# Performance work log

Measured on AMD Instinct MI355X. Metric: run time of the kernel, lower is better.

The kernel has to match this reference:

```python
import jax, jax.numpy as jnp
from jax import lax
import numpy as np

NE = 8          # ne_num
IDX_REF = 4     # ne_num // 2
EPS_BN = 1e-5


def conv2d(x, w, b=None, pad=0):
    out = lax.conv_general_dilated(x, w, (1, 1), [(pad, pad), (pad, pad)],
                                   dimension_numbers=('NCHW', 'OIHW', 'NCHW'))
    if b is not None:
        out = out + b[None, :, None, None]
    return out


def bn(x, gamma, beta):
    # training-mode batch norm (biased variance), as nn.BatchNorm2d in train()
    mu = x.mean(axis=(0, 2, 3), keepdims=True)
    var = x.var(axis=(0, 2, 3), keepdims=True)
    xn = (x - mu) * lax.rsqrt(var + EPS_BN)
    return xn * gamma[None, :, None, None] + beta[None, :, None, None]


def gauss_win(sigma):
    # sigma: (B,1). window_size=3 -> bias = [-1, 0, -1]; pop center of 3x3 -> (B,8)
    bias = jnp.array([-1.0, 0.0, -1.0], dtype=sigma.dtype)
    g = jnp.exp(bias[None, :] / (2.0 * sigma ** 2))            # (B,3)
    w1 = g / g.sum(axis=1, keepdims=True)                      # (B,3)
    w2 = (w1[:, :, None] * w1[:, None, :]).reshape(-1, 9)      # (B,9)
    return jnp.concatenate([w2[:, :4], w2[:, 5:]], axis=1)     # (B,8) center removed


def bilinear(img, y, x):
    # img: (B,H,W); y,x: (B,K,H,W) float sample coords; zero padding outside
    B, H, W = img.shape
    y0 = jnp.floor(y); x0 = jnp.floor(x)
    wy1 = y - y0; wy0 = 1.0 - wy1
    wx1 = x - x0; wx0 = 1.0 - wx1
    imgf = img.reshape(B, -1)

    def gather(yi, xi):
        yii = yi.astype(jnp.int32); xii = xi.astype(jnp.int32)
        valid = (yii >= 0) & (yii < H) & (xii >= 0) & (xii < W)
        idx = jnp.clip(yii, 0, H - 1) * W + jnp.clip(xii, 0, W - 1)
        v = jnp.take_along_axis(imgf, idx.reshape(B, -1), axis=1).reshape(idx.shape)
        return jnp.where(valid, v, 0.0)

    return (wy0 * wx0 * gather(y0, x0) + wy0 * wx1 * gather(y0, x0 + 1.0)
            + wy1 * wx0 * gather(y0 + 1.0, x0) + wy1 * wx1 * gather(y0 + 1.0, x0 + 1.0))


def modulated_deform_conv_1x9(fusion, offset, mask):
    # ModulatedDeformConvFunction with weight=ones(1,1,3,3), bias=0, stride=1,
    # pad=1, dilation=1, groups=1, deformable_groups=1.
    # fusion: (B,1,H,W); offset: (B,9,2,H,W) [per-neighbor (dy,dx)]; mask: (B,9,H,W)
    B, _, H, W = fusion.shape
    k = jnp.arange(9)
    py = (k // 3 - 1).astype(fusion.dtype)[None, :, None, None]
    px = (k % 3 - 1).astype(fusion.dtype)[None, :, None, None]
    hh = jnp.arange(H, dtype=fusion.dtype)[None, None, :, None]
    ww = jnp.arange(W, dtype=fusion.dtype)[None, None, None, :]
    y = hh + py + offset[:, :, 0]
    x = ww + px + offset[:, :, 1]
    samp = bilinear(fusion[:, 0], y, x)            # (B,9,H,W)
    return (mask * samp).sum(axis=1, keepdims=True)  # (B,1,H,W)


def _forward(feat, g1_w, g1_g, g1_b, g2_w, g2_g, g2_b, g3_w, g3_bias,
             f1_w, f1_g, f1_b, f2_w, f2_bias,
             s1_w, s1_b, s2_w, s2_b, s3_w, s3_b,
             oa1_w, oa1_g, oa1_b, oa2_w, oa2_g, oa2_b, oa3_w, oa3_bias,
             aff_scale):
    B, _, H, W = feat.shape
    # guid branch (5x5 convs)
    guid = jax.nn.relu(bn(conv2d(feat, g1_w, pad=2), g1_g, g1_b))
    guid = jax.nn.relu(bn(conv2d(guid, g2_w, pad=2), g2_g, g2_b))
    guid = conv2d(guid, g3_w, g3_bias, pad=2)                      # (B,8,H,W)
    # fuse branch
    f = jax.nn.relu(bn(conv2d(feat, f1_w, pad=1), f1_g, f1_b))
    fusion = jnp.tanh(conv2d(f, f2_w, f2_bias, pad=1))             # (B,1,H,W)
    # sigma branch (CAM, detached input)
    fd = lax.stop_gradient(feat)
    p = fd.mean(axis=(2, 3))                                       # (B,32)
    h = jax.nn.celu(p @ s1_w.T + s1_b)
    h = jax.nn.celu(h @ s2_w.T + s2_b)
    sigma = jax.nn.relu(h @ s3_w.T + s3_b) + 0.001                 # (B,1)
    # get_off_aff(guid, sigma, sigma_gamma=0.2, window_size=3)
    oa = jax.nn.relu(bn(conv2d(guid, oa1_w, pad=2), oa1_g, oa1_b))
    oa = jax.nn.relu(bn(conv2d(oa, oa2_w, pad=2), oa2_g, oa2_b))
    oa = conv2d(oa, oa3_w, oa3_bias, pad=2)                        # (B,24,H,W)
    o1, o2, affc = jnp.split(oa, 3, axis=1)                        # each (B,8,H,W)
    off = jnp.concatenate([o1, o2], axis=1).reshape(B, NE, 2, H, W)
    zero_ref = jnp.zeros((B, 1, 2, H, W), dtype=off.dtype)
    offset = jnp.concatenate([off[:, :IDX_REF], zero_ref, off[:, IDX_REF:]], axis=1)  # (B,9,2,H,W)
    gk = gauss_win(sigma + 0.2)                                    # (B,8)
    aff = jnp.tanh(affc) / (aff_scale + 1e-5) + gk[:, :, None, None]
    sa = jnp.abs(aff).sum(axis=1, keepdims=True) + 1e-5
    sa = jnp.maximum(sa, 1.0)
    aff = aff / sa
    aff_ref = 1.0 - aff.sum(axis=1, keepdims=True)
    aff9 = jnp.concatenate([aff[:, :IDX_REF], aff_ref, aff[:, IDX_REF:]], axis=1)  # (B,9,H,W)
    # gauss_filter (times=1) + abs
    gfusion = jnp.abs(modulated_deform_conv_1x9(fusion, offset, aff9))
    return gfusion


def setup_inputs() -> dict:
    key = jax.random.key(0)
    ks = list(jax.random.split(key, 32))
    B, C, H, W = 8, 32, 320, 320
    ne = NE
    d = {}
    d['feat'] = jax.random.normal(ks[0], (B, C, H, W), jnp.float32)

    def wconv(k, o, i, s):
        return jax.random.normal(k, (o, i, s, s), jnp.float32) * (1.0 / np.sqrt(i * s * s))

    def wlin(k, o, i):
        return jax.random.normal(k, (o, i), jnp.float32) * (1.0 / np.sqrt(i))

    # guid: 32->32 (5), 32->8 (5), 8->8 (5, bias)
    d['g1_w'] = wconv(ks[1], C, C, 5); d['g1_g'] = jnp.ones(C) + 0.1 * jax.random.normal(ks[2], (C,)); d['g1_b'] = 0.1 * jax.random.normal(ks[3], (C,))
    d['g2_w'] = wconv(ks[4], ne, C, 5); d['g2_g'] = jnp.ones(ne) + 0.1 * jax.random.normal(ks[5], (ne,)); d['g2_b'] = 0.1 * jax.random.normal(ks[6], (ne,))
    d['g3_w'] = wconv(ks[7], ne, ne, 5); d['g3_bias'] = 0.1 * jax.random.normal(ks[8], (ne,))
    # fuse: 32->32 (3), 32->1 (3, bias)
    d['f1_w'] = wconv(ks[9], C, C, 3); d['f1_g'] = jnp.ones(C) + 0.1 * jax.random.normal(ks[10], (C,)); d['f1_b'] = 0.1 * jax.random.normal(ks[11], (C,))
    d['f2_w'] = wconv(ks[12], 1, C, 3); d['f2_bias'] = 0.1 * jax.random.normal(ks[13], (1,))
    # gen_sigma CAM: 32->16->16->1
    d['s1_w'] = wlin(ks[14], 16, C); d['s1_b'] = 0.1 * jax.random.normal(ks[15], (16,))
    d['s2_w'] = wlin(ks[16], 16, 16); d['s2_b'] = 0.1 * jax.random.normal(ks[17], (16,))
    d['s3_w'] = wlin(ks[18], 1, 16); d['s3_b'] = 0.1 * jax.random.normal(ks[19], (1,))
    # conv_off_aff: 8->8 (5), 8->24 (5), 24->24 (5, bias)
    d['oa1_w'] = wconv(ks[20], ne, ne, 5); d['oa1_g'] = jnp.ones(ne) + 0.1 * jax.random.normal(ks[21], (ne,)); d['oa1_b'] = 0.1 * jax.random.normal(ks[22], (ne,))
    d['oa2_w'] = wconv(ks[23], 3 * ne, ne, 5); d['oa2_g'] = jnp.ones(3 * ne) + 0.1 * jax.random.normal(ks[24], (3 * ne,)); d['oa2_b'] = 0.1 * jax.random.normal(ks[25], (3 * ne,))
    d['oa3_w'] = wconv(ks[26], 3 * ne, 3 * ne, 5); d['oa3_bias'] = 0.1 * jax.random.normal(ks[27], (3 * ne,))
    # aff_scale_const = aff_gamma * ne_num = 0.5 * 8
    d['aff_scale'] = jnp.full((1,), 4.0, jnp.float32)
    return d


def reference(feat, g1_w, g1_g, g1_b, g2_w, g2_g, g2_b, g3_w, g3_bias,
              f1_w, f1_g, f1_b, f2_w, f2_bias,
              s1_w, s1_b, s2_w, s2_b, s3_w, s3_b,
              oa1_w, oa1_g, oa1_b, oa2_w, oa2_g, oa2_b, oa3_w, oa3_bias,
              aff_scale):
    return _forward(feat, g1_w, g1_g, g1_b, g2_w, g2_g, g2_b, g3_w, g3_bias,
                    f1_w, f1_g, f1_b, f2_w, f2_bias,
                    s1_w, s1_b, s2_w, s2_b, s3_w, s3_b,
                    oa1_w, oa1_g, oa1_b, oa2_w, oa2_g, oa2_b, oa3_w, oa3_bias,
                    aff_scale)
```

## Files before the change

### kernel.cpp

```cpp
#include <hip/hip_runtime.h>
#include <hip/hip_bf16.h>
#include <math.h>

#define B_   8
#define H_   320
#define W_   320
#define HW_  (320*320)

typedef __attribute__((ext_vector_type(8))) short bf16x8;
typedef __attribute__((ext_vector_type(4))) short bf16x4s;
typedef __attribute__((ext_vector_type(4))) float f32x4;

__device__ __forceinline__ short f2b(float v){
    __hip_bfloat16 h = __float2bfloat16(v);
    return *(short*)&h;
}
__device__ __forceinline__ float bf2f(short v){
    unsigned u = ((unsigned)(unsigned short)v) << 16;
    return __uint_as_float(u);
}

__global__ void convert_k(const float* __restrict__ in, short* __restrict__ out,
                          float* __restrict__ psum){
    const int b  = blockIdx.y;
    const int px = blockIdx.x*256 + threadIdx.x;
    const float* src = in + (long)b*32*HW_ + px;
    short* dst = out + ((long)b*HW_ + px)*32;
    float f[32];
    short v[32];
    #pragma unroll
    for (int c=0;c<32;++c){ f[c] = src[(long)c*HW_]; v[c] = f2b(f[c]); }
    #pragma unroll
    for (int s=0;s<4;++s)
        *(bf16x8*)(dst + s*8) = *(bf16x8*)(v + s*8);
    #pragma unroll
    for (int c=0;c<32;++c){
        float s = f[c];
        #pragma unroll
        for (int o=1;o<64;o<<=1) s += __shfl_xor(s, o, 64);
        f[c] = s;
    }
    __shared__ float red[4][32];
    const int lane = threadIdx.x & 63, wid = threadIdx.x >> 6;
    if (lane < 32) red[wid][lane] = f[lane];
    __syncthreads();
    if (threadIdx.x < 32)
        atomicAdd(&psum[b*32 + threadIdx.x],
                  red[0][threadIdx.x]+red[1][threadIdx.x]+red[2][threadIdx.x]+red[3][threadIdx.x]);
}

__global__ void repack_k(const float* __restrict__ sf1, const float* __restrict__ sf2,
                         const float* __restrict__ sg1, const float* __restrict__ sg2,
                         const float* __restrict__ sg3, const float* __restrict__ so1,
                         const float* __restrict__ so2, const float* __restrict__ so3,
                         short* __restrict__ dst){
    const int cum[8]  = {9216,13824,39424,52224,55808,59392,66560,92160};
    const int CINs[8] = {32,32,32,32, 8, 8, 8,24};
    const int CIps[8] = {32,32,32,32, 8, 8, 8,32};
    const int COUTs[8]= {32, 1,32, 8, 8, 8,24,24};
    const int MTs[8]  = { 2, 1, 2, 1, 1, 1, 2, 2};
    const int Ks[8]   = { 3, 3, 5, 5, 5, 5, 5, 5};
    int i = blockIdx.x*256 + threadIdx.x;
    if (i >= 92160) return;
    int s = 0;
    while (i >= cum[s]) ++s;
    const int base = s ? cum[s-1] : 0;
    const int il = i - base;
    const float* src = (s==0)?sf1:(s==1)?sf2:(s==2)?sg1:(s==3)?sg2:(s==4)?sg3:(s==5)?so1:(s==6)?so2:so3;
    const int kl   = il & 31;
    const int co_l = (il >> 5) & 15;
    const int rem  = il >> 9;
    const int MT = MTs[s];
    const int mt = rem % MT;
    const int c  = rem / MT;
    const int K = Ks[s];
    int tap, ci;
    if (CIps[s] == 32){ tap = (c % K)*K + (c / K); ci = kl; }
    else              { tap = c*4 + (kl>>3); ci = kl & 7; }
    const int co = mt*16 + co_l;
    float v = 0.f;
    if (co < COUTs[s] && ci < CINs[s] && tap < K*K){
        const int ky = tap / K, kx = tap - ky*K;
        v = src[((co*CINs[s] + ci)*K + ky)*K + kx];
    }
    dst[i] = f2b(v);
}

__device__ __forceinline__
float deform_px(const float* val, const float* __restrict__ fus_b,
                const float* __restrict__ gk_b, float inv_s, int y, int x){
    float aff[8]; float sa = 0.f;
    #pragma unroll
    for (int n=0;n<8;++n){
        float a = tanhf(val[16+n]) * inv_s + gk_b[n];
        aff[n] = a; sa += fabsf(a);
    }
    sa += 1e-5f;
    sa = fmaxf(sa, 1.f);
    const float isa = 1.f/sa;
    float ssum = 0.f;
    #pragma unroll
    for (int n=0;n<8;++n){ aff[n] *= isa; ssum += aff[n]; }
    const float aff_ref = 1.f - ssum;

    float o = 0.f;
    #pragma unroll
    for (int k=0;k<9;++k){
        float dy, dx, m;
        if (k == 4){ dy = 0.f; dx = 0.f; m = aff_ref; }
        else {
            const int n = (k < 4) ? k : k-1;
            dy = val[2*n];
            dx = val[2*n+1];
            m  = aff[n];
        }
        float yy = (float)(y + k/3 - 1) + dy;
        float xx = (float)(x + k%3 - 1) + dx;
        float y0f = floorf(yy), x0f = floorf(xx);
        int   y0 = (int)y0f,    x0i = (int)x0f;
        float wy1 = yy - y0f, wy0 = 1.f - wy1;
        float wx1 = xx - x0f, wx0 = 1.f - wx1;
        float v00 = (y0  >=0 && y0  <H_ && x0i  >=0 && x0i  <W_) ? fus_b[ y0   *W_ + x0i  ] : 0.f;
        float v01 = (y0  >=0 && y0  <H_ && x0i+1>=0 && x0i+1<W_) ? fus_b[ y0   *W_ + x0i+1] : 0.f;
        float v10 = (y0+1>=0 && y0+1<H_ && x0i  >=0 && x0i  <W_) ? fus_b[(y0+1)*W_ + x0i  ] : 0.f;
        float v11 = (y0+1>=0 && y0+1<H_ && x0i+1>=0 && x0i+1<W_) ? fus_b[(y0+1)*W_ + x0i+1] : 0.f;
        o += m * (wy0*(wx0*v00 + wx1*v01) + wy1*(wx0*v10 + wx1*v11));
    }
    return fabsf(o);
}

template<int CIN, int CIp, int COUT, int MT, int K,
         bool IN_BN, bool OUT_STATS, int OUT_MODE, int OCP>
__global__ __launch_bounds__(256, 4)
void mconv_k(const void* __restrict__ inv,
             const float* __restrict__ bn_sum, const float* __restrict__ bn_sq,
             const float* __restrict__ gamma, const float* __restrict__ beta,
             const short* __restrict__ wr, const float* __restrict__ bias,
             void* __restrict__ outv,
             float* __restrict__ osum, float* __restrict__ osq,
             const float* __restrict__ fus, const float* __restrict__ gk,
             const float* __restrict__ aff_scale){
    constexpr int PAD = K/2;
    constexpr int TH  = 8;
    constexpr int LW  = 32 + K - 1;
    constexpr int LH  = TH + K - 1;
    constexpr int SEGS = CIp/8;
    constexpr int PLANE = LH*LW*8 + 8;
    constexpr int NTAPS  = K*K;
    constexpr int NCHUNK = (CIp==32) ? NTAPS : (NTAPS*CIp + 31)/32;
    constexpr int INB  = (CIp==32) ? (SEGS*PLANE*2) : (LH*LW*8*2);
    constexpr int DUMPB = 256*25*4;
    constexpr int LDSB = (OUT_MODE==3 && INB < DUMPB) ? DUMPB : INB;

    __shared__ __align__(16) char ldsraw[LDSB];
    short* lds_in = (short*)ldsraw;
    __shared__ float sc_sh[2][32];
    __shared__ float red[2][4][32];

    const int tid = threadIdx.x;
    const int b   = blockIdx.z;
    const int x0  = blockIdx.x*32, y0 = blockIdx.y*TH;

    const int lane = tid & 63;
    const int wv   = tid >> 6;
    const int pxn  = lane & 15;
    const int quad = lane >> 4;
    const int row0 = 2*wv;

    if (IN_BN){
        if (tid < 32){
            float s = 1.f, sh2 = 0.f;
            if (tid < CIN){
                const float invN = 1.f/(float)(B_*HW_);
                float mu  = bn_sum[tid]*invN;
                float var = bn_sq[tid]*invN - mu*mu;
                s   = gamma[tid] * rsqrtf(var + 1e-5f);
                sh2 = beta[tid] - mu*s;
            }
            sc_sh[0][tid] = s;
            sc_sh[1][tid] = sh2;
        }
        __syncthreads();
    }

    constexpr int KC = (CIp==32) ? K : 1;
    bf16x8 aC[KC][MT];
    bf16x8 aAll[(CIp==8)?NCHUNK:1][MT];

    if constexpr (CIp == 32){
        #pragma unroll
        for (int ky=0; ky<K; ++ky)
            #pragma unroll
            for (int m=0;m<MT;++m)
                aC[ky][m] = *(const bf16x8*)(wr + ((ky*MT + m)*16 + pxn)*32 + quad*8);
    } else {
        #pragma unroll
        for (int c=0;c<NCHUNK;++c)
            #pragma unroll
            for (int m=0;m<MT;++m)
                aAll[c][m] = *(const bf16x8*)(wr + (((c*MT + m)*16 + pxn)*32 + quad*8));
    }

    {
        const short* src = (const short*)inv + (long)b*HW_*CIp;
        constexpr int NU = LH*LW*SEGS;
        constexpr int NIT = (NU + 255)/256;
        bf16x8 vv[NIT];
        int    la[NIT];
        bool   ib[NIT];
        #pragma unroll
        for (int it=0; it<NIT; ++it){
            const int u = tid + it*256;
            bf16x8 v = {0,0,0,0,0,0,0,0};
            bool inb = false;
            int addr = 0;
            if (u < NU){
                const int r   = u / (LW*SEGS);
                const int rem = u - r*(LW*SEGS);
                const int xl  = rem / SEGS;
                const int seg = rem - xl*SEGS;
                const int gy = y0 + r - PAD, gx = x0 + xl - PAD;
                addr = seg*PLANE + (r*LW + xl)*8;
                inb = (gy>=0 && gy<H_ && gx>=0 && gx<W_);
                if (inb)
                    v = *(const bf16x8*)(src + ((long)gy*W_ + gx)*CIp + seg*8);
            }
            vv[it] = v; la[it] = addr; ib[it] = inb;
        }
        __builtin_amdgcn_sched_barrier(0);
        #pragma unroll
        for (int it=0; it<NIT; ++it){
            const int u = tid + it*256;
            if (u < NU){
                bf16x8 v = vv[it];
                if (IN_BN && ib[it]){
                    const int seg = u - (u/SEGS)*SEGS;
                    #pragma unroll
                    for (int j=0;j<8;++j){
                        float f = bf2f(v[j]);
                        f = fmaxf(fmaf(f, sc_sh[0][seg*8+j], sc_sh[1][seg*8+j]), 0.f);
                        v[j] = f2b(f);
                    }
                }
                *(bf16x8*)&lds_in[la[it]] = v;
            }
        }
    }
    __syncthreads();

    const f32x4 zero = {0.f, 0.f, 0.f, 0.f};
    f32x4 acc[2][MT][2];
    #pragma unroll
    for (int rr=0;rr<2;++rr)
        #pragma unroll
        for (int m=0;m<MT;++m){ acc[rr][m][0] = zero; acc[rr][m][1] = zero; }

    if constexpr (CIp == 32){
        const short* bbase = lds_in + quad*PLANE + (row0*LW + pxn)*8;
        #pragma unroll
        for (int kx=0; kx<K; ++kx){
            bf16x8 bw[3][2];
            #pragma unroll
            for (int r=0;r<2;++r)
                #pragma unroll
                for (int n=0;n<2;++n)
                    bw[r][n] = *(const bf16x8*)(bbase + (r*LW + kx + n*16)*8);
            __builtin_amdgcn_sched_barrier(0);
            #pragma unroll
            for (int ky=0; ky<K; ++ky){
                if (ky < K-1){
                    #pragma unroll
                    for (int n=0;n<2;++n)
                        bw[(ky+2)%3][n] = *(const bf16x8*)(bbase + ((ky+2)*LW + kx + n*16)*8);
                }
                __builtin_amdgcn_sched_barrier(0);
                #pragma unroll
                for (int m=0;m<MT;++m){
                    acc[0][m][0] = __builtin_amdgcn_mfma_f32_16x16x32_bf16(aC[ky][m], bw[ky%3][0],     acc[0][m][0], 0,0,0);
                    acc[0][m][1] = __builtin_amdgcn_mfma_f32_16x16x32_bf16(aC[ky][m], bw[ky%3][1],     acc[0][m][1], 0,0,0);
                    acc[1][m][0] = __builtin_amdgcn_mfma_f32_16x16x32_bf16(aC[ky][m], bw[(ky+1)%3][0], acc[1][m][0], 0,0,0);
                    acc[1][m][1] = __builtin_amdgcn_mfma_f32_16x16x32_bf16(aC[ky][m], bw[(ky+1)%3][1], acc[1][m][1], 0,0,0);
                }
                if (kx+1 < K){
                    #pragma unroll
                    for (int m=0;m<MT;++m)
                        aC[ky][m] = *(const bf16x8*)(wr + ((((kx+1)*K+ky)*MT + m)*16 + pxn)*32 + quad*8);
                }
            }
        }
    } else {
        auto bptr = [&](int c, int rr)->const short*{
            const int row = row0 + rr;
            int t = c*4 + quad;
            if (t >= NTAPS) t = 0;
            const int ky = t / K, kx = t - ky*K;
            return lds_in + ((row+ky)*LW + kx + pxn)*8;
        };

        bf16x8 bcp[2][2][2];
        #pragma unroll
        for (int rr=0;rr<2;++rr){
            const short* bp = bptr(0, rr);
            bcp[0][rr][0] = *(const bf16x8*)bp;
            bcp[0][rr][1] = *(const bf16x8*)(bp + 16*8);
        }

        #pragma unroll
        for (int c=0; c<NCHUNK; ++c){
            if (c+1 < NCHUNK){
                #pragma unroll
                for (int rr=0;rr<2;++rr){
                    const short* bpn = bptr(c+1, rr);
                    bcp[(c+1)&1][rr][0] = *(const bf16x8*)bpn;
                    bcp[(c+1)&1][rr][1] = *(const bf16x8*)(bpn + 16*8);
                }
            }
            __builtin_amdgcn_sched_barrier(0);
            #pragma unroll
            for (int m=0;m<MT;++m)
                #pragma unroll
                for (int rr=0;rr<2;++rr){
                    acc[rr][m][0] = __builtin_amdgcn_mfma_f32_16x16x32_bf16(aAll[c][m], bcp[c&1][rr][0], acc[rr][m][0], 0,0,0);
                    acc[rr][m][1] = __builtin_amdgcn_mfma_f32_16x16x32_bf16(aAll[c][m], bcp[c&1][rr][1], acc[rr][m][1], 0,0,0);
                }
        }
    }

    if (OUT_STATS){
        #pragma unroll
        for (int m=0;m<MT;++m){
            #pragma unroll
            for (int r=0;r<4;++r){
                float v  = acc[0][m][0][r] + acc[0][m][1][r]
                         + acc[1][m][0][r] + acc[1][m][1][r];
                float v2 = acc[0][m][0][r]*acc[0][m][0][r] + acc[0][m][1][r]*acc[0][m][1][r]
                         + acc[1][m][0][r]*acc[1][m][0][r] + acc[1][m][1][r]*acc[1][m][1][r];
                #pragma unroll
                for (int o=1;o<16;o<<=1){
                    v  += __shfl_xor(v,  o, 64);
                    v2 += __shfl_xor(v2, o, 64);
                }
                if (pxn == 0){
                    red[0][wv][m*16 + quad*4 + r] = v;
                    red[1][wv][m*16 + quad*4 + r] = v2;
                }
            }
        }
        __syncthreads();
        if (tid < MT*16 && tid < COUT){
            atomicAdd(&osum[tid], red[0][0][tid]+red[0][1][tid]+red[0][2][tid]+red[0][3][tid]);
            atomicAdd(&osq[tid],  red[1][0][tid]+red[1][1][tid]+red[1][2][tid]+red[1][3][tid]);
        }
    }

    if (OUT_MODE == 3){
        float* out = (float*)outv;
        __syncthreads();
        float* dumpf = (float*)ldsraw;
        #pragma unroll
        for (int rr=0;rr<2;++rr){
            const int row = row0 + rr;
            #pragma unroll
            for (int m=0;m<MT;++m){
                if (m*16 + quad*4 < 24){
                    #pragma unroll
                    for (int n=0;n<2;++n)
                        #pragma unroll
                        for (int r=0;r<4;++r)
                            dumpf[(row*32 + n*16 + pxn)*25 + (m*16 + quad*4 + r)] = acc[rr][m][n][r];
                }
            }
        }
        __syncthreads();
        {
            float val[24];
            #pragma unroll
            for (int c2=0;c2<24;++c2) val[c2] = dumpf[tid*25 + c2] + bias[c2];
            const int yy = y0 + (tid>>5), xx = x0 + (tid&31);
            const float inv_s = 1.f/(aff_scale[0] + 1e-5f);
            out[(long)b*HW_ + yy*W_ + xx] =
                deform_px(val, fus + (long)b*HW_, gk + b*8, inv_s, yy, xx);
        }
    } else if (OUT_MODE == 2){
        float* out = (float*)outv;
        #pragma unroll
        for (int rr=0;rr<2;++rr){
            const int y = y0 + row0 + rr;
            #pragma unroll
            for (int m=0;m<MT;++m){
                #pragma unroll
                for (int r=0;r<4;++r){
                    const int co = m*16 + quad*4 + r;
                    if (co < COUT){
                        float* op = out + (((long)b*COUT + co)*H_ + y)*W_ + x0;
                        #pragma unroll
                        for (int n=0;n<2;++n)
                            op[n*16 + pxn] = tanhf(acc[rr][m][n][r] + bias[co]);
                    }
                }
            }
        }
    } else {
        short* o = (short*)outv;
        #pragma unroll
        for (int rr=0;rr<2;++rr){
            const int y = y0 + row0 + rr;
            #pragma unroll
            for (int m=0;m<MT;++m){
                const int co0 = m*16 + quad*4;
                if (co0 < OCP){
                    #pragma unroll
                    for (int n=0;n<2;++n){
                        bf16x4s pk;
                        #pragma unroll
                        for (int r=0;r<4;++r){
                            float f = acc[rr][m][n][r];
                            if (OUT_MODE == 1) f += bias[co0+r];
                            pk[r] = f2b(f);
                        }
                        const long px = ((long)b*H_ + y)*W_ + x0 + n*16 + pxn;
                        *(bf16x4s*)(o + px*OCP + co0) = pk;
                    }
                }
            }
        }
    }
}

template<int KK, int OFF>
__device__ __forceinline__
void conv_core32(const short* __restrict__ lds_in, const short* __restrict__ wr,
                 int row0, int pxn, int quad, f32x4 acc[2][2][2]){
    constexpr int LW = 36;
    constexpr int PLANE = 12*36*8 + 8;
    const short* bbase = lds_in + quad*PLANE + ((row0+OFF)*LW + OFF + pxn)*8;
    bf16x8 aC[KK][2];
    #pragma unroll
    for (int ky=0; ky<KK; ++ky)
        #pragma unroll
        for (int m=0;m<2;++m)
            aC[ky][m] = *(const bf16x8*)(wr + ((ky*2 + m)*16 + pxn)*32 + quad*8);
    #pragma unroll
    for (int kx=0; kx<KK; ++kx){
        bf16x8 bw[3][2];
        #pragma unroll
        for (int r=0;r<2;++r)
            #pragma unroll
            for (int n=0;n<2;++n)
                bw[r][n] = *(const bf16x8*)(bbase + (r*LW + kx + n*16)*8);
        __builtin_amdgcn_sched_barrier(0);
        #pragma unroll
        for (int ky=0; ky<KK; ++ky){
            if (ky < KK-1){
                #pragma unroll
                for (int n=0;n<2;++n)
                    bw[(ky+2)%3][n] = *(const bf16x8*)(bbase + ((ky+2)*LW + kx + n*16)*8);
            }
            __builtin_amdgcn_sched_barrier(0);
            #pragma unroll
            for (int m=0;m<2;++m){
                acc[0][m][0] = __builtin_amdgcn_mfma_f32_16x16x32_bf16(aC[ky][m], bw[ky%3][0],     acc[0][m][0], 0,0,0);
                acc[0][m][1] = __builtin_amdgcn_mfma_f32_16x16x32_bf16(aC[ky][m], bw[ky%3][1],     acc[0][m][1], 0,0,0);
                acc[1][m][0] = __builtin_amdgcn_mfma_f32_16x16x32_bf16(aC[ky][m], bw[(ky+1)%3][0], acc[1][m][0], 0,0,0);
                acc[1][m][1] = __builtin_amdgcn_mfma_f32_16x16x32_bf16(aC[ky][m], bw[(ky+1)%3][1], acc[1][m][1], 0,0,0);
            }
            if (kx+1 < KK){
                #pragma unroll
                for (int m=0;m<2;++m)
                    aC[ky][m] = *(const bf16x8*)(wr + ((((kx+1)*KK+ky)*2 + m)*16 + pxn)*32 + quad*8);
            }
        }
    }
}

__global__ __launch_bounds__(256, 4)
void mconv_fg_k(const short* __restrict__ feat,
                const short* __restrict__ wf, const short* __restrict__ wg,
                short* __restrict__ f1o, short* __restrict__ g1o,
                float* __restrict__ sum0, float* __restrict__ sq0,
                float* __restrict__ sum1, float* __restrict__ sq1){
    constexpr int PAD = 2, LW = 36, LH = 12, SEGS = 4;
    constexpr int PLANE = LH*LW*8 + 8;

    __shared__ __align__(16) char ldsraw[SEGS*PLANE*2];
    short* lds_in = (short*)ldsraw;
    __shared__ float red[2][4][32];

    const int tid = threadIdx.x;
    const int b   = blockIdx.z;
    const int x0  = blockIdx.x*32, y0 = blockIdx.y*8;

    const int lane = tid & 63;
    const int wv   = tid >> 6;
    const int pxn  = lane & 15;
    const int quad = lane >> 4;
    const int row0 = 2*wv;

    {
        const short* src = feat + (long)b*HW_*32;
        constexpr int NU = LH*LW*SEGS;
        constexpr int NIT = (NU + 255)/256;
        bf16x8 vv[NIT];
        int    la[NIT];
        #pragma unroll
        for (int it=0; it<NIT; ++it){
            const int u = tid + it*256;
            bf16x8 v = {0,0,0,0,0,0,0,0};
            int addr = 0;
            if (u < NU){
                const int r   = u / (LW*SEGS);
                const int rem = u - r*(LW*SEGS);
                const int xl  = rem / SEGS;
                const int seg = rem - xl*SEGS;
                const int gy = y0 + r - PAD, gx = x0 + xl - PAD;
                addr = seg*PLANE + (r*LW + xl)*8;
                if (gy>=0 && gy<H_ && gx>=0 && gx<W_)
                    v = *(const bf16x8*)(src + ((long)gy*W_ + gx)*32 + seg*8);
            }
            vv[it] = v; la[it] = addr;
        }
        __builtin_amdgcn_sched_barrier(0);
        #pragma unroll
        for (int it=0; it<NIT; ++it){
            if (tid + it*256 < NU)
                *(bf16x8*)&lds_in[la[it]] = vv[it];
        }
    }
    __syncthreads();

    const f32x4 zero = {0.f, 0.f, 0.f, 0.f};
    f32x4 acc[2][2][2];

    #pragma unroll
    for (int rr=0;rr<2;++rr)
        #pragma unroll
        for (int m=0;m<2;++m){ acc[rr][m][0] = zero; acc[rr][m][1] = zero; }
    conv_core32<3,1>(lds_in, wf, row0, pxn, quad, acc);
    #pragma unroll
    for (int m=0;m<2;++m)
        #pragma unroll
        for (int r=0;r<4;++r){
            float v  = acc[0][m][0][r] + acc[0][m][1][r] + acc[1][m][0][r] + acc[1][m][1][r];
            float v2 = acc[0][m][0][r]*acc[0][m][0][r] + acc[0][m][1][r]*acc[0][m][1][r]
                     + acc[1][m][0][r]*acc[1][m][0][r] + acc[1][m][1][r]*acc[1][m][1][r];
            #pragma unroll
            for (int o=1;o<16;o<<=1){ v += __shfl_xor(v, o, 64); v2 += __shfl_xor(v2, o, 64); }
            if (pxn == 0){ red[0][wv][m*16+quad*4+r] = v; red[1][wv][m*16+quad*4+r] = v2; }
        }
    __syncthreads();
    if (tid < 32){
        atomicAdd(&sum0[tid], red[0][0][tid]+red[0][1][tid]+red[0][2][tid]+red[0][3][tid]);
        atomicAdd(&sq0[tid],  red[1][0][tid]+red[1][1][tid]+red[1][2][tid]+red[1][3][tid]);
    }
    #pragma unroll
    for (int rr=0;rr<2;++rr){
        const int y = y0 + row0 + rr;
        #pragma unroll
        for (int m=0;m<2;++m){
            const int co0 = m*16 + quad*4;
            #pragma unroll
            for (int n=0;n<2;++n){
                bf16x4s pk;
                #pragma unroll
                for (int r=0;r<4;++r) pk[r] = f2b(acc[rr][m][n][r]);
                const long px = ((long)b*H_ + y)*W_ + x0 + n*16 + pxn;
                *(bf16x4s*)(f1o + px*32 + co0) = pk;
            }
        }
    }
    __syncthreads();

    #pragma unroll
    for (int rr=0;rr<2;++rr)
        #pragma unroll
        for (int m=0;m<2;++m){ acc[rr][m][0] = zero; acc[rr][m][1] = zero; }
    conv_core32<5,0>(lds_in, wg, row0, pxn, quad, acc);
    #pragma unroll
    for (int m=0;m<2;++m)
        #pragma unroll
        for (int r=0;r<4;++r){
            float v  = acc[0][m][0][r] + acc[0][m][1][r] + acc[1][m][0][r] + acc[1][m][1][r];
            float v2 = acc[0][m][0][r]*acc[0][m][0][r] + acc[0][m][1][r]*acc[0][m][1][r]
                     + acc[1][m][0][r]*acc[1][m][0][r] + acc[1][m][1][r]*acc[1][m][1][r];
            #pragma unroll
            for (int o=1;o<16;o<<=1){ v += __shfl_xor(v, o, 64); v2 += __shfl_xor(v2, o, 64); }
            if (pxn == 0){ red[0][wv][m*16+quad*4+r] = v; red[1][wv][m*16+quad*4+r] = v2; }
        }
    __syncthreads();
    if (tid < 32){
        atomicAdd(&sum1[tid], red[0][0][tid]+red[0][1][tid]+red[0][2][tid]+red[0][3][tid]);
        atomicAdd(&sq1[tid],  red[1][0][tid]+red[1][1][tid]+red[1][2][tid]+red[1][3][tid]);
    }
    #pragma unroll
    for (int rr=0;rr<2;++rr){
        const int y = y0 + row0 + rr;
        #pragma unroll
        for (int m=0;m<2;++m){
            const int co0 = m*16 + quad*4;
            #pragma unroll
            for (int n=0;n<2;++n){
                bf16x4s pk;
                #pragma unroll
                for (int r=0;r<4;++r) pk[r] = f2b(acc[rr][m][n][r]);
                const long px = ((long)b*H_ + y)*W_ + x0 + n*16 + pxn;
                *(bf16x4s*)(g1o + px*32 + co0) = pk;
            }
        }
    }
}

__global__ void sigma_k(const float* __restrict__ p,
                        const float* s1w, const float* s1b,
                        const float* s2w, const float* s2b,
                        const float* s3w, const float* s3b,
                        float* __restrict__ gk){
    const int b = threadIdx.x;
    if (b >= B_) return;
    float pb[32];
    for (int j=0;j<32;++j) pb[j] = p[b*32+j] * (1.f/(float)HW_);
    float h1[16], h2[16];
    for (int i=0;i<16;++i){
        float t = s1b[i];
        for (int j=0;j<32;++j) t = fmaf(pb[j], s1w[i*32+j], t);
        h1[i] = t > 0.f ? t : expm1f(t);
    }
    for (int i=0;i<16;++i){
        float t = s2b[i];
        for (int j=0;j<16;++j) t = fmaf(h1[j], s2w[i*16+j], t);
        h2[i] = t > 0.f ? t : expm1f(t);
    }
    float t = s3b[0];
    for (int j=0;j<16;++j) t = fmaf(h2[j], s3w[j], t);
    float sigma = fmaxf(t, 0.f) + 0.001f;
    float sg = sigma + 0.2f;
    float e = expf(-1.f/(2.f*sg*sg));
    float inv = 1.f/(2.f*e + 1.f);
    float a = e*inv, c = inv;
    float* g = gk + b*8;
    g[0]=a*a; g[1]=a*c; g[2]=a*a; g[3]=c*a; g[4]=c*a; g[5]=a*a; g[6]=a*c; g[7]=a*a;
}

extern "C" void kernel_launch(void* const* d_in, const int* in_sizes, int n_in,
                              void* d_out, int out_size, void* d_ws, size_t ws_size,
                              hipStream_t stream){
    const float* feat    = (const float*)d_in[0];
    const float* g1_w    = (const float*)d_in[1];
    const float* g1_g    = (const float*)d_in[2];
    const float* g1_b    = (const float*)d_in[3];
    const float* g2_w    = (const float*)d_in[4];
    const float* g2_g    = (const float*)d_in[5];
    const float* g2_b    = (const float*)d_in[6];
    const float* g3_w    = (const float*)d_in[7];
    const float* g3_bias = (const float*)d_in[8];
    const float* f1_w    = (const float*)d_in[9];
    const float* f1_g    = (const float*)d_in[10];
    const float* f1_b    = (const float*)d_in[11];
    const float* f2_w    = (const float*)d_in[12];
    const float* f2_bias = (const float*)d_in[13];
    const float* s1w     = (const float*)d_in[14];
    const float* s1b     = (const float*)d_in[15];
    const float* s2w     = (const float*)d_in[16];
    const float* s2b     = (const float*)d_in[17];
    const float* s3w     = (const float*)d_in[18];
    const float* s3b     = (const float*)d_in[19];
    const float* oa1_w   = (const float*)d_in[20];
    const float* oa1_g   = (const float*)d_in[21];
    const float* oa1_b   = (const float*)d_in[22];
    const float* oa2_w   = (const float*)d_in[23];
    const float* oa2_g   = (const float*)d_in[24];
    const float* oa2_b   = (const float*)d_in[25];
    const float* oa3_w   = (const float*)d_in[26];
    const float* oa3_bias= (const float*)d_in[27];
    const float* aff_scale=(const float*)d_in[28];
    float* out = (float*)d_out;

    char* ws = (char*)d_ws;
    short* FEAT = (short*)(ws + 0L);
    short* A1   = (short*)(ws + 52428800L);
    short* A2   = (short*)(ws + 104857600L);
    short* GUID = (short*)(ws + 117964800L);
    float* FUS  = (float*)(ws + 131072000L);
    float* SM   = (float*)(ws + 134348800L);
    short* OA2  = A1;
    short* G1O  = (short*)(ws + 135266304L);
    const bool merged = (ws_size >= 135266304UL + 52428800UL);

    float* sum = SM;
    float* sq  = SM + 320;
    float* p   = SM + 640;
    float* gk  = SM + 896;
    short* WBs = (short*)(SM + 960);
    short* w_f1 = WBs + 0;
    short* w_f2 = WBs + 9216;
    short* w_g1 = WBs + 13824;
    short* w_g2 = WBs + 39424;
    short* w_g3 = WBs + 52224;
    short* w_o1 = WBs + 55808;
    short* w_o2 = WBs + 59392;
    short* w_o3 = WBs + 66560;

    hipMemsetAsync(sum, 0, 896*sizeof(float), stream);

    repack_k<<<dim3(360), dim3(256), 0, stream>>>(
        f1_w, f2_w, g1_w, g2_w, g3_w, oa1_w, oa2_w, oa3_w, WBs);
    convert_k<<<dim3(HW_/256, B_), dim3(256), 0, stream>>>(feat, FEAT, p);

    sigma_k<<<dim3(1), dim3(64), 0, stream>>>(p, s1w, s1b, s2w, s2b, s3w, s3b, gk);

    const dim3 cgrid(10, 40, 8), cblk(256);
    #define MCONV(CIN,CIp,COUT,MT,K,IBN,OST,OM,OCP) \
        mconv_k<CIN,CIp,COUT,MT,K,IBN,OST,OM,OCP><<<cgrid,cblk,0,stream>>>

    const short* G1SRC;
    if (merged){
        mconv_fg_k<<<cgrid, cblk, 0, stream>>>(FEAT, w_f1, w_g1, A1, G1O,
                                               sum+0*64, sq+0*64, sum+1*64, sq+1*64);
        MCONV(32,32, 1,1,3,true ,false,2, 0)(A1, sum+0*64, sq+0*64, f1_g, f1_b,
            w_f2, f2_bias, FUS, nullptr, nullptr, nullptr, nullptr, nullptr);
        G1SRC = G1O;
    } else {
        MCONV(32,32,32,2,3,false,true ,0,32)(FEAT, nullptr, nullptr, nullptr, nullptr,
            w_f1, nullptr, A1, sum+0*64, sq+0*64, nullptr, nullptr, nullptr);
        MCONV(32,32, 1,1,3,true ,false,2, 0)(A1, sum+0*64, sq+0*64, f1_g, f1_b,
            w_f2, f2_bias, FUS, nullptr, nullptr, nullptr, nullptr, nullptr);
        MCONV(32,32,32,2,5,false,true ,0,32)(FEAT, nullptr, nullptr, nullptr, nullptr,
            w_g1, nullptr, A1, sum+1*64, sq+1*64, nullptr, nullptr, nullptr);
        G1SRC = A1;
    }

    MCONV(32,32, 8,1,5,true ,true ,0, 8)(G1SRC, sum+1*64, sq+1*64, g1_g, g1_b,
        w_g2, nullptr, A2, sum+2*64, sq+2*64, nullptr, nullptr, nullptr);
    MCONV( 8, 8, 8,1,5,true ,false,1, 8)(A2, sum+2*64, sq+2*64, g2_g, g2_b,
        w_g3, g3_bias, GUID, nullptr, nullptr, nullptr, nullptr, nullptr);

    MCONV( 8, 8, 8,1,5,false,true ,0, 8)(GUID, nullptr, nullptr, nullptr, nullptr,
        w_o1, nullptr, A2, sum+3*64, sq+3*64, nullptr, nullptr, nullptr);
    MCONV( 8, 8,24,2,5,true ,true ,0,32)(A2, sum+3*64, sq+3*64, oa1_g, oa1_b,
        w_o2, nullptr, OA2, sum+4*64, sq+4*64, nullptr, nullptr, nullptr);
    MCONV(24,32,24,2,5,true ,false,3, 0)(OA2, sum+4*64, sq+4*64, oa2_g, oa2_b,
        w_o3, oa3_bias, out, nullptr, nullptr, FUS, gk, aff_scale);
    #undef MCONV
}
```

Before: 567.4 us.

## Fuse fp32-to-bf16 input conversion and channel pooling into merged first conv

Removes the separate convert_k pass. The merged f1/g1 conv kernel now reads fp32 NCHW features directly, converts them to bf16 into LDS, and accumulates per-channel sums for sigma through shared and global atomics. The G1O buffer moves to the start of the workspace, freed now that the FEAT staging buffer is gone, which lowers the workspace size needed to take the merged path. The cost is strided per-channel global loads (32 scattered reads per pixel) in place of 16-byte vector loads, plus many LDS atomics per block.

```diff
diff --git a/kernel.cpp b/kernel.cpp
--- a/kernel.cpp
+++ b/kernel.cpp
@@ -474,17 +474,19 @@
 }
 
 __global__ __launch_bounds__(256, 4)
-void mconv_fg_k(const short* __restrict__ feat,
+void mconv_fg_k(const float* __restrict__ featf,
                 const short* __restrict__ wf, const short* __restrict__ wg,
                 short* __restrict__ f1o, short* __restrict__ g1o,
                 float* __restrict__ sum0, float* __restrict__ sq0,
-                float* __restrict__ sum1, float* __restrict__ sq1){
-    constexpr int PAD = 2, LW = 36, LH = 12, SEGS = 4;
+                float* __restrict__ sum1, float* __restrict__ sq1,
+                float* __restrict__ psum){
+    constexpr int PAD = 2, LW = 36, LH = 12;
     constexpr int PLANE = LH*LW*8 + 8;
 
-    __shared__ __align__(16) char ldsraw[SEGS*PLANE*2];
+    __shared__ __align__(16) char ldsraw[4*PLANE*2];
     short* lds_in = (short*)ldsraw;
     __shared__ float red[2][4][32];
+    __shared__ float psl[32];
 
     const int tid = threadIdx.x;
     const int b   = blockIdx.z;
@@ -496,37 +498,44 @@
     const int quad = lane >> 4;
     const int row0 = 2*wv;
 
+    if (tid < 32) psl[tid] = 0.f;
+    __syncthreads();
+
     {
-        const short* src = feat + (long)b*HW_*32;
-        constexpr int NU = LH*LW*SEGS;
-        constexpr int NIT = (NU + 255)/256;
-        bf16x8 vv[NIT];
-        int    la[NIT];
-        #pragma unroll
-        for (int it=0; it<NIT; ++it){
-            const int u = tid + it*256;
-            bf16x8 v = {0,0,0,0,0,0,0,0};
-            int addr = 0;
-            if (u < NU){
-                const int r   = u / (LW*SEGS);
-                const int rem = u - r*(LW*SEGS);
-                const int xl  = rem / SEGS;
-                const int seg = rem - xl*SEGS;
-                const int gy = y0 + r - PAD, gx = x0 + xl - PAD;
-                addr = seg*PLANE + (r*LW + xl)*8;
-                if (gy>=0 && gy<H_ && gx>=0 && gx<W_)
-                    v = *(const bf16x8*)(src + ((long)gy*W_ + gx)*32 + seg*8);
-            }
-            vv[it] = v; la[it] = addr;
-        }
-        __builtin_amdgcn_sched_barrier(0);
-        #pragma unroll
-        for (int it=0; it<NIT; ++it){
-            if (tid + it*256 < NU)
-                *(bf16x8*)&lds_in[la[it]] = vv[it];
+        const float* srcb = featf + (long)b*32*HW_;
+        #pragma unroll
+        for (int it=0; it<2; ++it){
+            const int upx = tid + it*256;
+            const bool valid = upx < LH*LW;
+            const int r  = valid ? (upx / LW) : 0;
+            const int xl = upx - r*LW;
+            const int gy = y0 + r - PAD, gx = x0 + xl - PAD;
+            const bool inb = valid && gy>=0 && gy<H_ && gx>=0 && gx<W_;
+            float f[32];
+            if (inb){
+                const float* sp = srcb + (long)gy*W_ + gx;
+                #pragma unroll
+                for (int c=0;c<32;++c) f[c] = sp[(long)c*HW_];
+            } else {
+                #pragma unroll
+                for (int c=0;c<32;++c) f[c] = 0.f;
+            }
+            if (valid){
+                short v[32];
+                #pragma unroll
+                for (int c=0;c<32;++c) v[c] = f2b(f[c]);
+                #pragma unroll
+                for (int s=0;s<4;++s)
+                    *(bf16x8*)&lds_in[s*PLANE + (r*LW + xl)*8] = *(bf16x8*)(v + s*8);
+            }
+            if (valid && r>=PAD && r<PAD+8 && xl>=PAD && xl<PAD+32){
+                #pragma unroll
+                for (int c=0;c<32;++c) atomicAdd(&psl[c], f[c]);
+            }
         }
     }
     __syncthreads();
+    if (tid < 32) atomicAdd(&psum[b*32 + tid], psl[tid]);
 
     const f32x4 zero = {0.f, 0.f, 0.f, 0.f};
     f32x4 acc[2][2][2];
@@ -682,8 +691,8 @@
     float* FUS  = (float*)(ws + 131072000L);
     float* SM   = (float*)(ws + 134348800L);
     short* OA2  = A1;
-    short* G1O  = (short*)(ws + 135266304L);
-    const bool merged = (ws_size >= 135266304UL + 52428800UL);
+    short* G1O  = (short*)(ws + 0L);
+    const bool merged = (ws_size >= 134348800UL + 4096UL*400UL);
 
     float* sum = SM;
     float* sq  = SM + 320;
@@ -703,9 +712,6 @@
 
     repack_k<<<dim3(360), dim3(256), 0, stream>>>(
         f1_w, f2_w, g1_w, g2_w, g3_w, oa1_w, oa2_w, oa3_w, WBs);
-    convert_k<<<dim3(HW_/256, B_), dim3(256), 0, stream>>>(feat, FEAT, p);
-
-    sigma_k<<<dim3(1), dim3(64), 0, stream>>>(p, s1w, s1b, s2w, s2b, s3w, s3b, gk);
 
     const dim3 cgrid(10, 40, 8), cblk(256);
     #define MCONV(CIN,CIp,COUT,MT,K,IBN,OST,OM,OCP) \
@@ -713,12 +719,15 @@
 
     const short* G1SRC;
     if (merged){
-        mconv_fg_k<<<cgrid, cblk, 0, stream>>>(FEAT, w_f1, w_g1, A1, G1O,
-                                               sum+0*64, sq+0*64, sum+1*64, sq+1*64);
+        mconv_fg_k<<<cgrid, cblk, 0, stream>>>(feat, w_f1, w_g1, A1, G1O,
+                                               sum+0*64, sq+0*64, sum+1*64, sq+1*64, p);
+        sigma_k<<<dim3(1), dim3(64), 0, stream>>>(p, s1w, s1b, s2w, s2b, s3w, s3b, gk);
         MCONV(32,32, 1,1,3,true ,false,2, 0)(A1, sum+0*64, sq+0*64, f1_g, f1_b,
             w_f2, f2_bias, FUS, nullptr, nullptr, nullptr, nullptr, nullptr);
         G1SRC = G1O;
     } else {
+        convert_k<<<dim3(HW_/256, B_), dim3(256), 0, stream>>>(feat, FEAT, p);
+        sigma_k<<<dim3(1), dim3(64), 0, stream>>>(p, s1w, s1b, s2w, s2b, s3w, s3b, gk);
         MCONV(32,32,32,2,3,false,true ,0,32)(FEAT, nullptr, nullptr, nullptr, nullptr,
             w_f1, nullptr, A1, sum+0*64, sq+0*64, nullptr, nullptr, nullptr);
         MCONV(32,32, 1,1,3,true ,false,2, 0)(A1, sum+0*64, sq+0*64, f1_g, f1_b,
```

After: 821.0 us. +44.7%, slower.
